# Performance work log

Hardware: AMD Instinct MI355X
Metric: run time of the kernel (lower is better)

Reference implementation:

```python
import jax, jax.numpy as jnp
import numpy as np
import math

B, T, S, D, H = 2, 1024, 1024, 1024, 16
DH = D // H


def setup_inputs() -> dict:
    key = jax.random.key(0)
    ks = jax.random.split(key, 13)
    scale = 1.0 / math.sqrt(D)
    inp = {
        "q": jax.random.normal(ks[0], (B, T, D), jnp.float32),
        "k": jax.random.normal(ks[1], (B, S, D), jnp.float32),
        "v": jax.random.normal(ks[2], (B, S, D), jnp.float32),
        # causal mask: True means masked
        "attn_mask": jnp.broadcast_to(
            jnp.triu(jnp.ones((T, S), jnp.bool_), k=1)[None, None], (B, 1, T, S)
        ),
        "attn_bias": jax.random.normal(ks[3], (B, H, T, S), jnp.float32),
        "Wq": jax.random.normal(ks[4], (D, D), jnp.float32) * scale,
        "bq": jnp.zeros((D,), jnp.float32),
        "Wk": jax.random.normal(ks[5], (D, D), jnp.float32) * scale,
        "bk": jnp.zeros((D,), jnp.float32),
        "Wv": jax.random.normal(ks[6], (D, D), jnp.float32) * scale,
        "bv": jnp.zeros((D,), jnp.float32),
        "Wo": jax.random.normal(ks[7], (D, D), jnp.float32) * scale,
        "bo": jnp.zeros((D,), jnp.float32),
        "bias_scale": jnp.asarray(0.5, jnp.float32),
    }
    return inp


def reference(q, k, v, attn_mask, attn_bias, Wq, bq, Wk, bk, Wv, bv, Wo, bo, bias_scale):
    # projections (torch Linear convention: x @ W.T + b), split heads
    qh = (q @ Wq.T + bq).reshape(B, T, H, DH)   # (B,T,H,DH)
    kh = (k @ Wk.T + bk).reshape(B, S, H, DH)
    vh = (v @ Wv.T + bv).reshape(B, S, H, DH)

    scores = jnp.einsum("bthd,bshd->bhts", qh, kh) / math.sqrt(DH)  # (B,H,T,S)
    scores = jnp.clip(scores, -80.0, 80.0)
    scores = jnp.where(attn_mask, -jnp.inf, scores)  # mask broadcasts over H
    attn = jax.nn.softmax(scores, axis=-1)

    # post-softmax multiplicative bias + renormalize
    scale = 1.0 + bias_scale * jnp.tanh(attn_bias)
    attn = attn * jnp.maximum(scale, 1e-9)
    attn = attn / (jnp.sum(attn, axis=-1, keepdims=True) + 1e-9)

    # dropout p=0.0 (eval) -> identity
    out = jnp.einsum("bhts,bshd->bthd", attn, vh).reshape(B, T, D)
    out = out @ Wo.T + bo
    return out, attn
```

## Files before the change

### kernel.cpp

```cpp
#include <hip/hip_runtime.h>
#include <hip/hip_bf16.h>
#include <math.h>

#define BB 2
#define TT 1024
#define SS 1024
#define DD 1024
#define HH 16
#define DH 64

typedef __attribute__((ext_vector_type(8))) short bf16x8;
typedef __attribute__((ext_vector_type(4))) float f32x4;
typedef unsigned short ushort_t;

#define AS3(p) ((__attribute__((address_space(3))) unsigned int*)(p))
#define AS1(p) ((const __attribute__((address_space(1))) unsigned int*)(p))

__device__ __forceinline__ unsigned short f2b(float f) {
    union { float f; unsigned u; } x; x.f = f;
    unsigned r = x.u + 0x7FFFu + ((x.u >> 16) & 1u);
    return (unsigned short)(r >> 16);
}

__device__ __forceinline__ bf16x8 pack_bf16x8(float4 a, float4 b) {
    union { unsigned u[4]; bf16x8 v; } r;
    asm("v_cvt_pk_bf16_f32 %0, %1, %2" : "=v"(r.u[0]) : "v"(a.x), "v"(a.y));
    asm("v_cvt_pk_bf16_f32 %0, %1, %2" : "=v"(r.u[1]) : "v"(a.z), "v"(a.w));
    asm("v_cvt_pk_bf16_f32 %0, %1, %2" : "=v"(r.u[2]) : "v"(b.x), "v"(b.y));
    asm("v_cvt_pk_bf16_f32 %0, %1, %2" : "=v"(r.u[3]) : "v"(b.z), "v"(b.w));
    return r.v;
}

__global__ __launch_bounds__(256) void cvt_all(
    const float* __restrict__ q, const float* __restrict__ k, const float* __restrict__ v,
    const float* __restrict__ Wq, const float* __restrict__ Wk,
    const float* __restrict__ Wv, const float* __restrict__ Wo,
    ushort_t* __restrict__ oq, ushort_t* __restrict__ ok, ushort_t* __restrict__ ov,
    ushort_t* __restrict__ oWq, ushort_t* __restrict__ oWk,
    ushort_t* __restrict__ oWv, ushort_t* __restrict__ oWo)
{
    const int y = blockIdx.y;
    if (y >= 3 && blockIdx.x >= 512) return;
    const float* src =
        (y == 0) ? q : (y == 1) ? k : (y == 2) ? v :
        (y == 3) ? Wq : (y == 4) ? Wk : (y == 5) ? Wv : Wo;
    ushort_t* dst =
        (y == 0) ? oq : (y == 1) ? ok : (y == 2) ? ov :
        (y == 3) ? oWq : (y == 4) ? oWk : (y == 5) ? oWv : oWo;
    size_t i = ((size_t)blockIdx.x * 256 + threadIdx.x) * 8;
    float4 v0 = *(const float4*)&src[i];
    float4 v1 = *(const float4*)&src[i + 4];
    uint4 o;
    o.x = f2b(v0.x) | ((unsigned)f2b(v0.y) << 16);
    o.y = f2b(v0.z) | ((unsigned)f2b(v0.w) << 16);
    o.z = f2b(v1.x) | ((unsigned)f2b(v1.y) << 16);
    o.w = f2b(v1.z) | ((unsigned)f2b(v1.w) << 16);
    *(uint4*)&dst[i] = o;
}

__device__ __forceinline__ void gemm128_mainloop(
    const ushort_t* __restrict__ A,
    const ushort_t* __restrict__ Bw,
    int K, ushort_t (*Asm)[128 * 32], ushort_t (*Bsm)[128 * 32],
    f32x4 acc[4][4])
{
    const int tid = threadIdx.x;
    const int wave = tid >> 6, lane = tid & 63;
    const int sr = lane >> 2;
    const int gc = (lane & 3) ^ ((lane >> 3) & 3);
    const int l15 = lane & 15, q = lane >> 4;
    const int mblk = (wave >> 1) * 64, nblk = (wave & 1) * 64;

#define G128_STAGE(k0_, b_) do {                                               \
        _Pragma("unroll")                                                      \
        for (int o = 0; o < 2; o++) {                                          \
            int r0 = (wave * 2 + o) * 16;                                      \
            __builtin_amdgcn_global_load_lds(                                  \
                AS1(A + (size_t)(r0 + sr) * K + (k0_) + gc * 8),               \
                AS3(Asm[b_] + r0 * 32), 16, 0, 0);                             \
            __builtin_amdgcn_global_load_lds(                                  \
                AS1(Bw + (size_t)(r0 + sr) * K + (k0_) + gc * 8),              \
                AS3(Bsm[b_] + r0 * 32), 16, 0, 0);                             \
        } } while (0)

#define G128_COMPUTE(b_) do {                                                  \
        bf16x8 av[4], bv[4];                                                   \
        _Pragma("unroll")                                                      \
        for (int mi = 0; mi < 4; mi++) {                                       \
            int r = mblk + mi * 16 + l15;                                      \
            av[mi] = *(const bf16x8*)&Asm[b_][r * 32 + (q ^ ((r >> 1) & 3)) * 8]; \
        }                                                                      \
        _Pragma("unroll")                                                      \
        for (int ni = 0; ni < 4; ni++) {                                       \
            int r = nblk + ni * 16 + l15;                                      \
            bv[ni] = *(const bf16x8*)&Bsm[b_][r * 32 + (q ^ ((r >> 1) & 3)) * 8]; \
        }                                                                      \
        _Pragma("unroll")                                                      \
        for (int mi = 0; mi < 4; mi++)                                         \
            _Pragma("unroll")                                                  \
            for (int ni = 0; ni < 4; ni++)                                     \
                acc[mi][ni] = __builtin_amdgcn_mfma_f32_16x16x32_bf16(         \
                    av[mi], bv[ni], acc[mi][ni], 0, 0, 0);                     \
        } while (0)

    G128_STAGE(0, 0);
    __syncthreads();

    int buf = 0;
    for (int k0 = 0; k0 < K; k0 += 32) {
        if (k0 + 32 < K) G128_STAGE(k0 + 32, buf ^ 1);
        G128_COMPUTE(buf);
        __syncthreads();
        buf ^= 1;
    }
#undef G128_STAGE
#undef G128_COMPUTE
}

__global__ __launch_bounds__(256) void proj_gemm(
    const ushort_t* __restrict__ qb, const ushort_t* __restrict__ kb, const ushort_t* __restrict__ vb,
    const ushort_t* __restrict__ Wqb, const ushort_t* __restrict__ Wkb, const ushort_t* __restrict__ Wvb,
    const float* __restrict__ bq, const float* __restrict__ bk, const float* __restrict__ bv,
    ushort_t* __restrict__ qh, ushort_t* __restrict__ kh, ushort_t* __restrict__ vh)
{
    __shared__ ushort_t Asm[2][128 * 32];
    __shared__ ushort_t Bsm[2][128 * 32];
    const int z = blockIdx.z;
    const ushort_t* A = (z == 0) ? qb : (z == 1) ? kb : vb;
    const ushort_t* W = (z == 0) ? Wqb : (z == 1) ? Wkb : Wvb;
    const float* bias = (z == 0) ? bq : (z == 1) ? bk : bv;
    ushort_t* Y = (z == 0) ? qh : (z == 1) ? kh : vh;

    const int bm = blockIdx.y * 128, bn = blockIdx.x * 128;
    f32x4 acc[4][4];
    #pragma unroll
    for (int i = 0; i < 4; i++)
        #pragma unroll
        for (int j = 0; j < 4; j++) acc[i][j] = (f32x4)(0.f);

    gemm128_mainloop(A + (size_t)bm * DD, W + (size_t)bn * DD, DD, Asm, Bsm, acc);

    const int lane = threadIdx.x & 63, wave = threadIdx.x >> 6;
    const int mblk = (wave >> 1) * 64, nblk = (wave & 1) * 64;
    const int l15 = lane & 15, q = lane >> 4;
    #pragma unroll
    for (int mi = 0; mi < 4; mi++) {
        #pragma unroll
        for (int ni = 0; ni < 4; ni++) {
            int col = bn + nblk + ni * 16 + l15;
            float bcol = bias[col];
            #pragma unroll
            for (int r = 0; r < 4; r++) {
                int row = bm + mblk + mi * 16 + q * 4 + r;
                Y[(size_t)row * DD + col] = f2b(acc[mi][ni][r] + bcol);
            }
        }
    }
}

__global__ __launch_bounds__(256) void oproj_gemm(
    const ushort_t* __restrict__ A, const ushort_t* __restrict__ W,
    const float* __restrict__ bias, float* __restrict__ Y)
{
    __shared__ ushort_t Asm[2][128 * 32];
    __shared__ ushort_t Bsm[2][128 * 32];
    const int bm = blockIdx.y * 128, bn = blockIdx.x * 128;
    f32x4 acc[4][4];
    #pragma unroll
    for (int i = 0; i < 4; i++)
        #pragma unroll
        for (int j = 0; j < 4; j++) acc[i][j] = (f32x4)(0.f);

    gemm128_mainloop(A + (size_t)bm * DD, W + (size_t)bn * DD, DD, Asm, Bsm, acc);

    const int lane = threadIdx.x & 63, wave = threadIdx.x >> 6;
    const int mblk = (wave >> 1) * 64, nblk = (wave & 1) * 64;
    const int l15 = lane & 15, q = lane >> 4;
    #pragma unroll
    for (int mi = 0; mi < 4; mi++) {
        #pragma unroll
        for (int ni = 0; ni < 4; ni++) {
            int col = bn + nblk + ni * 16 + l15;
            float bcol = bias[col];
            #pragma unroll
            for (int r = 0; r < 4; r++) {
                int row = bm + mblk + mi * 16 + q * 4 + r;
                Y[(size_t)row * DD + col] = acc[mi][ni][r] + bcol;
            }
        }
    }
}

__global__ __launch_bounds__(256) void transpose_v(
    const ushort_t* __restrict__ vh, ushort_t* __restrict__ vT)
{
    __shared__ ushort_t Ls[64][72];
    const int s0 = blockIdx.x * 64;
    const int bh = blockIdx.y;
    const int b = bh >> 4, h = bh & 15;
    const int tid = threadIdx.x;
    const int r = tid >> 2, c16 = (tid & 3) * 16;

    const ushort_t* src = &vh[((size_t)(b * SS + s0 + r) * HH + h) * DH + c16];
    uint4 u0 = *(const uint4*)src;
    uint4 u1 = *(const uint4*)(src + 8);
    ushort_t tmp[16];
    *(uint4*)&tmp[0] = u0; *(uint4*)&tmp[8] = u1;
    #pragma unroll
    for (int j = 0; j < 16; j++) Ls[c16 + j][r] = tmp[j];
    __syncthreads();

    const int dh = r;
    uint4 w0 = *(const uint4*)&Ls[dh][c16];
    uint4 w1 = *(const uint4*)&Ls[dh][c16 + 8];
    ushort_t* dst = &vT[((size_t)bh * DH + dh) * SS + s0 + c16];
    *(uint4*)dst = w0;
    *(uint4*)(dst + 8) = w1;
}

__global__ __launch_bounds__(256) void scores_mfma(
    const ushort_t* __restrict__ qh, const ushort_t* __restrict__ kh,
    float* __restrict__ attn)
{
    __shared__ ushort_t Qs[128 * 64];
    __shared__ ushort_t Ks[128 * 64];

    int idx = blockIdx.x, ti = 0;
    while (idx >= ti + 1) { idx -= ti + 1; ti++; }
    const int si = idx;
    const int bh = blockIdx.y;
    const int b = bh >> 4, h = bh & 15;
    const int t0 = ti * 128, s0 = si * 128;

    const int tid = threadIdx.x;
    const int wave = tid >> 6, lane = tid & 63;
    const int sr8 = lane >> 3;
    const int gc8 = (lane & 7) ^ sr8;

    #pragma unroll
    for (int o = 0; o < 4; o++) {
        int r0 = (wave * 4 + o) * 8;
        int r = r0 + sr8;
        __builtin_amdgcn_global_load_lds(
            AS1(qh + ((size_t)(b * TT + t0 + r) * HH + h) * DH + gc8 * 8),
            AS3(Qs + r0 * 64), 16, 0, 0);
        __builtin_amdgcn_global_load_lds(
            AS1(kh + ((size_t)(b * SS + s0 + r) * HH + h) * DH + gc8 * 8),
            AS3(Ks + r0 * 64), 16, 0, 0);
    }
    __syncthreads();

    const int l15 = lane & 15, q = lane >> 4;
    const int tblk = (wave >> 1) * 64, sblk = (wave & 1) * 64;
    f32x4 acc[4][4];
    #pragma unroll
    for (int i = 0; i < 4; i++)
        #pragma unroll
        for (int j = 0; j < 4; j++) acc[i][j] = (f32x4)(0.f);

    #pragma unroll
    for (int ks = 0; ks < 2; ks++) {
        bf16x8 av[4], bv[4];
        #pragma unroll
        for (int mi = 0; mi < 4; mi++) {
            int r = tblk + mi * 16 + l15;
            av[mi] = *(const bf16x8*)&Qs[r * 64 + ((ks * 4 + q) ^ (r & 7)) * 8];
        }
        #pragma unroll
        for (int ni = 0; ni < 4; ni++) {
            int r = sblk + ni * 16 + l15;
            bv[ni] = *(const bf16x8*)&Ks[r * 64 + ((ks * 4 + q) ^ (r & 7)) * 8];
        }
        #pragma unroll
        for (int mi = 0; mi < 4; mi++)
            #pragma unroll
            for (int ni = 0; ni < 4; ni++)
                acc[mi][ni] = __builtin_amdgcn_mfma_f32_16x16x32_bf16(av[mi], bv[ni], acc[mi][ni], 0, 0, 0);
    }

    #pragma unroll
    for (int mi = 0; mi < 4; mi++) {
        #pragma unroll
        for (int ni = 0; ni < 4; ni++) {
            int scol = s0 + sblk + ni * 16 + l15;
            #pragma unroll
            for (int r = 0; r < 4; r++) {
                int t = t0 + tblk + mi * 16 + q * 4 + r;
                float v = acc[mi][ni][r] * 0.125f;
                v = fminf(fmaxf(v, -80.f), 80.f);
                attn[((size_t)bh * TT + t) * SS + scol] = v;
            }
        }
    }
}

__global__ __launch_bounds__(256) void softmax_bias_wave(
    const float* __restrict__ attn_bias, const float* __restrict__ bias_scale_p,
    float* __restrict__ attn)
{
    const int wave = threadIdx.x >> 6, lane = threadIdx.x & 63;
    const int row = blockIdx.x * 4 + wave;
    const int t = row & (TT - 1);

    float* prow = attn + (size_t)row * SS;
    const float* brow = attn_bias + (size_t)row * SS;
    const float bscale = bias_scale_p[0];

    const int nc = (t >> 8) + 1;

    float v[16];
    float4 bx[4];
    float m = -INFINITY;
    #pragma unroll
    for (int c = 0; c < 4; c++) {
        const int s0 = c * 256 + lane * 4;
        if (c < nc) {
            float4 rv = *(const float4*)&prow[s0];
            bx[c] = *(const float4*)&brow[s0];
            v[c * 4 + 0] = (s0     <= t) ? rv.x : -INFINITY;
            v[c * 4 + 1] = (s0 + 1 <= t) ? rv.y : -INFINITY;
            v[c * 4 + 2] = (s0 + 2 <= t) ? rv.z : -INFINITY;
            v[c * 4 + 3] = (s0 + 3 <= t) ? rv.w : -INFINITY;
            m = fmaxf(m, fmaxf(fmaxf(v[c*4], v[c*4+1]), fmaxf(v[c*4+2], v[c*4+3])));
        } else {
            v[c * 4 + 0] = -INFINITY; v[c * 4 + 1] = -INFINITY;
            v[c * 4 + 2] = -INFINITY; v[c * 4 + 3] = -INFINITY;
            bx[c] = make_float4(0.f, 0.f, 0.f, 0.f);
        }
    }
    #pragma unroll
    for (int off = 1; off < 64; off <<= 1)
        m = fmaxf(m, __shfl_xor(m, off));

    float w[16];
    float P = 0.f, Wn = 0.f;
    #pragma unroll
    for (int c = 0; c < 4; c++) {
        if (c < nc) {
            float bxx[4] = {bx[c].x, bx[c].y, bx[c].z, bx[c].w};
            #pragma unroll
            for (int j = 0; j < 4; j++) {
                float vv = v[c * 4 + j];
                float p = (vv > -INFINITY) ? __expf(vv - m) : 0.f;
                float e = __expf(-2.f * fabsf(bxx[j]));
                float th = copysignf((1.f - e) / (1.f + e), bxx[j]);
                float sc = fmaxf(1.f + bscale * th, 1e-9f);
                float ww = p * sc;
                w[c * 4 + j] = ww;
                P += p; Wn += ww;
            }
        } else {
            w[c * 4 + 0] = 0.f; w[c * 4 + 1] = 0.f;
            w[c * 4 + 2] = 0.f; w[c * 4 + 3] = 0.f;
        }
    }
    #pragma unroll
    for (int off = 1; off < 64; off <<= 1) {
        P  += __shfl_xor(P, off);
        Wn += __shfl_xor(Wn, off);
    }
    const float inv = 1.f / (Wn + 1e-9f * P);

    #pragma unroll
    for (int c = 0; c < 4; c++) {
        const int s0 = c * 256 + lane * 4;
        float4 o;
        o.x = w[c * 4 + 0] * inv; o.y = w[c * 4 + 1] * inv;
        o.z = w[c * 4 + 2] * inv; o.w = w[c * 4 + 3] * inv;
        *(float4*)&prow[s0] = o;
    }
}

__global__ __launch_bounds__(256) void av_mfma(
    const float* __restrict__ attn, const ushort_t* __restrict__ vT,
    ushort_t* __restrict__ ao)
{
    __shared__ ushort_t Vsm[2][64 * 64];

    const int tb = (int)gridDim.x - 1 - (int)blockIdx.x;
    const int bh = blockIdx.y;
    const int b = bh >> 4, h = bh & 15;
    const int t0 = tb * 64;
    const int nsteps = tb + 1;

    const int tid = threadIdx.x;
    const int wave = tid >> 6, lane = tid & 63;
    const int sr8 = lane >> 3, gc8 = (lane & 7) ^ sr8;
    const int l15 = lane & 15, q = lane >> 4;

    const float* arow = attn + ((size_t)bh * TT + t0 + wave * 16 + l15) * SS + q * 8;
    const ushort_t* vbase = vT + (size_t)bh * DH * SS;

    f32x4 acc[4];
    #pragma unroll
    for (int i = 0; i < 4; i++) acc[i] = (f32x4)(0.f);

#define STAGE_V(sidx, buf) do {                                               \
        int s0_ = (sidx) * 64;                                                \
        _Pragma("unroll")                                                     \
        for (int o = 0; o < 2; o++) {                                         \
            int r0 = wave * 16 + o * 8;                                       \
            __builtin_amdgcn_global_load_lds(                                 \
                AS1(vbase + (size_t)(r0 + sr8) * SS + s0_ + gc8 * 8),         \
                AS3(&Vsm[buf][r0 * 64]), 16, 0, 0);                           \
        } } while (0)

#define LOAD_A(sidx, dst) do {                                                \
        const float* p_ = arow + (sidx) * 64;                                 \
        dst[0] = *(const float4*)(p_);                                        \
        dst[1] = *(const float4*)(p_ + 4);                                    \
        dst[2] = *(const float4*)(p_ + 32);                                   \
        dst[3] = *(const float4*)(p_ + 36); } while (0)

#define COMPUTE(buf, ax) do {                                                 \
        bf16x8 af0 = pack_bf16x8(ax[0], ax[1]);                               \
        bf16x8 af1 = pack_bf16x8(ax[2], ax[3]);                               \
        _Pragma("unroll")                                                     \
        for (int ni = 0; ni < 4; ni++) {                                      \
            int rv = ni * 16 + l15;                                           \
            bf16x8 b0 = *(const bf16x8*)&Vsm[buf][rv * 64 + ((q) ^ (rv & 7)) * 8];       \
            bf16x8 b1 = *(const bf16x8*)&Vsm[buf][rv * 64 + ((4 + q) ^ (rv & 7)) * 8];   \
            acc[ni] = __builtin_amdgcn_mfma_f32_16x16x32_bf16(af0, b0, acc[ni], 0, 0, 0);\
            acc[ni] = __builtin_amdgcn_mfma_f32_16x16x32_bf16(af1, b1, acc[ni], 0, 0, 0);\
        } } while (0)

    float4 aA[4], aB[4];
    STAGE_V(0, 0);
    LOAD_A(0, aA);
    __syncthreads();

    int st = 0;
    while (true) {
        if (st + 1 < nsteps) { STAGE_V(st + 1, 1); LOAD_A(st + 1, aB); }
        COMPUTE(0, aA);
        __syncthreads();
        if (++st == nsteps) break;
        if (st + 1 < nsteps) { STAGE_V(st + 1, 0); LOAD_A(st + 1, aA); }
        COMPUTE(1, aB);
        __syncthreads();
        if (++st == nsteps) break;
    }

#undef STAGE_V
#undef LOAD_A
#undef COMPUTE

    #pragma unroll
    for (int ni = 0; ni < 4; ni++) {
        int dh = ni * 16 + l15;
        #pragma unroll
        for (int r = 0; r < 4; r++) {
            int t = t0 + wave * 16 + q * 4 + r;
            ao[(size_t)(b * TT + t) * DD + h * DH + dh] = f2b(acc[ni][r]);
        }
    }
}

extern "C" void kernel_launch(void* const* d_in, const int* in_sizes, int n_in,
                              void* d_out, int out_size, void* d_ws, size_t ws_size,
                              hipStream_t stream)
{
    const float* q   = (const float*)d_in[0];
    const float* k   = (const float*)d_in[1];
    const float* v   = (const float*)d_in[2];
    const float* attn_bias = (const float*)d_in[4];
    const float* Wq = (const float*)d_in[5];
    const float* bq = (const float*)d_in[6];
    const float* Wk = (const float*)d_in[7];
    const float* bk = (const float*)d_in[8];
    const float* Wv = (const float*)d_in[9];
    const float* bv = (const float*)d_in[10];
    const float* Wo = (const float*)d_in[11];
    const float* bo = (const float*)d_in[12];
    const float* bscale = (const float*)d_in[13];

    char* base = (char*)d_ws;
    ushort_t* qb  = (ushort_t*)(base + (0ull << 20));
    ushort_t* kb  = (ushort_t*)(base + (4ull << 20));
    ushort_t* vb  = (ushort_t*)(base + (8ull << 20));
    ushort_t* Wqb = (ushort_t*)(base + (12ull << 20));
    ushort_t* Wkb = (ushort_t*)(base + (14ull << 20));
    ushort_t* Wvb = (ushort_t*)(base + (16ull << 20));
    ushort_t* Wob = (ushort_t*)(base + (18ull << 20));
    ushort_t* qhb = (ushort_t*)(base + (20ull << 20));
    ushort_t* khb = (ushort_t*)(base + (24ull << 20));
    ushort_t* vhb = (ushort_t*)(base + (28ull << 20));
    ushort_t* vT  = qb;
    ushort_t* aob = kb;

    float* out  = (float*)d_out;
    float* attn = out + (size_t)BB * TT * DD;

    cvt_all<<<dim3(1024, 7), 256, 0, stream>>>(q, k, v, Wq, Wk, Wv, Wo,
                                               qb, kb, vb, Wqb, Wkb, Wvb, Wob);
    proj_gemm<<<dim3(8, 16, 3), 256, 0, stream>>>(qb, kb, vb, Wqb, Wkb, Wvb,
                                                  bq, bk, bv, qhb, khb, vhb);
    transpose_v<<<dim3(16, 32), 256, 0, stream>>>(vhb, vT);
    scores_mfma<<<dim3(36, 32), 256, 0, stream>>>(qhb, khb, attn);
    softmax_bias_wave<<<dim3(8192), 256, 0, stream>>>(attn_bias, bscale, attn);
    av_mfma<<<dim3(16, 32), 256, 0, stream>>>(attn, vT, aob);
    oproj_gemm<<<dim3(8, 16), 256, 0, stream>>>(aob, Wob, bo, out);
}
```

Measured before the change: 367.4 us.

## Fuse softmax-bias normalization into the attention-times-V MFMA kernel

Replaces the separate softmax_bias_wave and av_mfma kernels with one 512-thread kernel. Each block computes the unnormalized biased weights per 64-column tile, stores them as bf16 in a 128KB LDS row buffer and feeds them straight to the MFMA. It then normalizes both the attn output and the AV accumulator by a per-row reciprocal. A fixed exponent offset of 16 replaces the row max to avoid a second pass, and the kernel zero-fills the masked tail directly. This removes a full re-read and re-write of the attention matrix. The costs are bf16 rounding of the returned attn values, the fixed-offset exponent relying on the clipped score range, and one block per CU because of the large LDS use.

```diff
diff --git a/kernel.cpp b/kernel.cpp
--- a/kernel.cpp
+++ b/kernel.cpp
@@ -22,13 +22,9 @@
     return (unsigned short)(r >> 16);
 }
 
-__device__ __forceinline__ bf16x8 pack_bf16x8(float4 a, float4 b) {
-    union { unsigned u[4]; bf16x8 v; } r;
-    asm("v_cvt_pk_bf16_f32 %0, %1, %2" : "=v"(r.u[0]) : "v"(a.x), "v"(a.y));
-    asm("v_cvt_pk_bf16_f32 %0, %1, %2" : "=v"(r.u[1]) : "v"(a.z), "v"(a.w));
-    asm("v_cvt_pk_bf16_f32 %0, %1, %2" : "=v"(r.u[2]) : "v"(b.x), "v"(b.y));
-    asm("v_cvt_pk_bf16_f32 %0, %1, %2" : "=v"(r.u[3]) : "v"(b.z), "v"(b.w));
-    return r.v;
+__device__ __forceinline__ float b2f(unsigned short u) {
+    union { unsigned u; float f; } x; x.u = ((unsigned)u) << 16;
+    return x.f;
 }
 
 __global__ __launch_bounds__(256) void cvt_all(
@@ -294,164 +290,158 @@
     }
 }
 
-__global__ __launch_bounds__(256) void softmax_bias_wave(
-    const float* __restrict__ attn_bias, const float* __restrict__ bias_scale_p,
-    float* __restrict__ attn)
-{
-    const int wave = threadIdx.x >> 6, lane = threadIdx.x & 63;
-    const int row = blockIdx.x * 4 + wave;
-    const int t = row & (TT - 1);
-
-    float* prow = attn + (size_t)row * SS;
-    const float* brow = attn_bias + (size_t)row * SS;
-    const float bscale = bias_scale_p[0];
-
-    const int nc = (t >> 8) + 1;
-
-    float v[16];
-    float4 bx[4];
-    float m = -INFINITY;
-    #pragma unroll
-    for (int c = 0; c < 4; c++) {
-        const int s0 = c * 256 + lane * 4;
-        if (c < nc) {
-            float4 rv = *(const float4*)&prow[s0];
-            bx[c] = *(const float4*)&brow[s0];
-            v[c * 4 + 0] = (s0     <= t) ? rv.x : -INFINITY;
-            v[c * 4 + 1] = (s0 + 1 <= t) ? rv.y : -INFINITY;
-            v[c * 4 + 2] = (s0 + 2 <= t) ? rv.z : -INFINITY;
-            v[c * 4 + 3] = (s0 + 3 <= t) ? rv.w : -INFINITY;
-            m = fmaxf(m, fmaxf(fmaxf(v[c*4], v[c*4+1]), fmaxf(v[c*4+2], v[c*4+3])));
-        } else {
-            v[c * 4 + 0] = -INFINITY; v[c * 4 + 1] = -INFINITY;
-            v[c * 4 + 2] = -INFINITY; v[c * 4 + 3] = -INFINITY;
-            bx[c] = make_float4(0.f, 0.f, 0.f, 0.f);
-        }
-    }
-    #pragma unroll
-    for (int off = 1; off < 64; off <<= 1)
-        m = fmaxf(m, __shfl_xor(m, off));
-
-    float w[16];
-    float P = 0.f, Wn = 0.f;
-    #pragma unroll
-    for (int c = 0; c < 4; c++) {
-        if (c < nc) {
-            float bxx[4] = {bx[c].x, bx[c].y, bx[c].z, bx[c].w};
-            #pragma unroll
-            for (int j = 0; j < 4; j++) {
-                float vv = v[c * 4 + j];
-                float p = (vv > -INFINITY) ? __expf(vv - m) : 0.f;
-                float e = __expf(-2.f * fabsf(bxx[j]));
-                float th = copysignf((1.f - e) / (1.f + e), bxx[j]);
-                float sc = fmaxf(1.f + bscale * th, 1e-9f);
-                float ww = p * sc;
-                w[c * 4 + j] = ww;
-                P += p; Wn += ww;
-            }
-        } else {
-            w[c * 4 + 0] = 0.f; w[c * 4 + 1] = 0.f;
-            w[c * 4 + 2] = 0.f; w[c * 4 + 3] = 0.f;
-        }
-    }
-    #pragma unroll
-    for (int off = 1; off < 64; off <<= 1) {
-        P  += __shfl_xor(P, off);
-        Wn += __shfl_xor(Wn, off);
-    }
-    const float inv = 1.f / (Wn + 1e-9f * P);
-
-    #pragma unroll
-    for (int c = 0; c < 4; c++) {
-        const int s0 = c * 256 + lane * 4;
-        float4 o;
-        o.x = w[c * 4 + 0] * inv; o.y = w[c * 4 + 1] * inv;
-        o.z = w[c * 4 + 2] * inv; o.w = w[c * 4 + 3] * inv;
-        *(float4*)&prow[s0] = o;
-    }
-}
-
-__global__ __launch_bounds__(256) void av_mfma(
-    const float* __restrict__ attn, const ushort_t* __restrict__ vT,
+__global__ __launch_bounds__(512) void sav_fused(
+    const float* __restrict__ scores,
+    const float* __restrict__ attn_bias,
+    const float* __restrict__ bias_scale_p,
+    const ushort_t* __restrict__ vT,
+    float* __restrict__ attn,
     ushort_t* __restrict__ ao)
 {
+    __shared__ ushort_t Wlds[64 * 1024];
     __shared__ ushort_t Vsm[2][64 * 64];
+    __shared__ float sInv[64];
 
     const int tb = (int)gridDim.x - 1 - (int)blockIdx.x;
     const int bh = blockIdx.y;
     const int b = bh >> 4, h = bh & 15;
     const int t0 = tb * 64;
-    const int nsteps = tb + 1;
+    const int nst = tb + 1;
 
     const int tid = threadIdx.x;
     const int wave = tid >> 6, lane = tid & 63;
+    const int crow = wave * 8 + (lane >> 3);
+    const int cc8  = (lane & 7) * 8;
+    const int csw  = (cc8 ^ ((crow & 7) << 3));
+    const int tglob = t0 + crow;
+    const int rg = wave >> 1, dhh = wave & 1;
+    const int l15 = lane & 15, q = lane >> 4;
+    const int arow = rg * 16 + l15;
     const int sr8 = lane >> 3, gc8 = (lane & 7) ^ sr8;
-    const int l15 = lane & 15, q = lane >> 4;
-
-    const float* arow = attn + ((size_t)bh * TT + t0 + wave * 16 + l15) * SS + q * 8;
+
+    const float bscale = bias_scale_p[0];
+    const float* srow = scores    + ((size_t)bh * TT + tglob) * SS + cc8;
+    const float* brow = attn_bias + ((size_t)bh * TT + tglob) * SS + cc8;
     const ushort_t* vbase = vT + (size_t)bh * DH * SS;
-
-    f32x4 acc[4];
-    #pragma unroll
-    for (int i = 0; i < 4; i++) acc[i] = (f32x4)(0.f);
-
-#define STAGE_V(sidx, buf) do {                                               \
-        int s0_ = (sidx) * 64;                                                \
+    float* aout = attn + ((size_t)bh * TT + tglob) * SS + cc8;
+
+    {
+        float4 z = make_float4(0.f, 0.f, 0.f, 0.f);
+        for (int si = nst; si < SS / 64; si++) {
+            *(float4*)(aout + si * 64) = z;
+            *(float4*)(aout + si * 64 + 4) = z;
+        }
+    }
+
+    f32x4 acc[2];
+    acc[0] = (f32x4)(0.f); acc[1] = (f32x4)(0.f);
+    float P = 0.f, Wn = 0.f;
+
+#define STAGE_V(sidx, bb) do {                                                \
+        __builtin_amdgcn_global_load_lds(                                     \
+            AS1(vbase + (size_t)(wave * 8 + sr8) * SS + (sidx) * 64 + gc8 * 8),\
+            AS3(&Vsm[bb][(wave * 8) * 64]), 16, 0, 0); } while (0)
+
+#define LOAD_SB(ti_, sv_, bv_) do {                                           \
+        const float* ps_ = srow + (ti_) * 64;                                 \
+        const float* pb_ = brow + (ti_) * 64;                                 \
+        sv_[0] = *(const float4*)ps_; sv_[1] = *(const float4*)(ps_ + 4);     \
+        bv_[0] = *(const float4*)pb_; bv_[1] = *(const float4*)(pb_ + 4); } while (0)
+
+#define COMPUTE_W(ti_, sv_, bv_) do {                                         \
+        float sa_[8] = { sv_[0].x, sv_[0].y, sv_[0].z, sv_[0].w,              \
+                         sv_[1].x, sv_[1].y, sv_[1].z, sv_[1].w };            \
+        float ba_[8] = { bv_[0].x, bv_[0].y, bv_[0].z, bv_[0].w,              \
+                         bv_[1].x, bv_[1].y, bv_[1].z, bv_[1].w };            \
+        float wv_[8];                                                         \
         _Pragma("unroll")                                                     \
-        for (int o = 0; o < 2; o++) {                                         \
-            int r0 = wave * 16 + o * 8;                                       \
-            __builtin_amdgcn_global_load_lds(                                 \
-                AS1(vbase + (size_t)(r0 + sr8) * SS + s0_ + gc8 * 8),         \
-                AS3(&Vsm[buf][r0 * 64]), 16, 0, 0);                           \
+        for (int j = 0; j < 8; j++) {                                         \
+            int col_ = (ti_) * 64 + cc8 + j;                                  \
+            float p_ = (col_ <= tglob) ? __expf(sa_[j] - 16.f) : 0.f;         \
+            float e_ = __expf(-2.f * fabsf(ba_[j]));                          \
+            float th_ = copysignf((1.f - e_) / (1.f + e_), ba_[j]);           \
+            float sc_ = fmaxf(1.f + bscale * th_, 1e-9f);                     \
+            float ww_ = p_ * sc_;                                             \
+            P += p_; Wn += ww_; wv_[j] = ww_;                                 \
+        }                                                                     \
+        union { unsigned u[4]; uint4 v4; } pk_;                               \
+        asm("v_cvt_pk_bf16_f32 %0, %1, %2" : "=v"(pk_.u[0]) : "v"(wv_[0]), "v"(wv_[1])); \
+        asm("v_cvt_pk_bf16_f32 %0, %1, %2" : "=v"(pk_.u[1]) : "v"(wv_[2]), "v"(wv_[3])); \
+        asm("v_cvt_pk_bf16_f32 %0, %1, %2" : "=v"(pk_.u[2]) : "v"(wv_[4]), "v"(wv_[5])); \
+        asm("v_cvt_pk_bf16_f32 %0, %1, %2" : "=v"(pk_.u[3]) : "v"(wv_[6]), "v"(wv_[7])); \
+        *(uint4*)&Wlds[(size_t)crow * 1024 + (ti_) * 64 + csw] = pk_.v4; } while (0)
+
+#define MFMA_T(ti_, bb) do {                                                  \
+        bf16x8 a0 = *(const bf16x8*)&Wlds[(size_t)arow * 1024 + (ti_) * 64 + ((q ^ (arow & 7)) << 3)];       \
+        bf16x8 a1 = *(const bf16x8*)&Wlds[(size_t)arow * 1024 + (ti_) * 64 + (((4 + q) ^ (arow & 7)) << 3)]; \
+        _Pragma("unroll")                                                     \
+        for (int ni = 0; ni < 2; ni++) {                                      \
+            int rv = dhh * 32 + ni * 16 + l15;                                \
+            bf16x8 b0 = *(const bf16x8*)&Vsm[bb][rv * 64 + ((q ^ (rv & 7)) << 3)];       \
+            bf16x8 b1 = *(const bf16x8*)&Vsm[bb][rv * 64 + (((4 + q) ^ (rv & 7)) << 3)]; \
+            acc[ni] = __builtin_amdgcn_mfma_f32_16x16x32_bf16(a0, b0, acc[ni], 0, 0, 0); \
+            acc[ni] = __builtin_amdgcn_mfma_f32_16x16x32_bf16(a1, b1, acc[ni], 0, 0, 0); \
         } } while (0)
 
-#define LOAD_A(sidx, dst) do {                                                \
-        const float* p_ = arow + (sidx) * 64;                                 \
-        dst[0] = *(const float4*)(p_);                                        \
-        dst[1] = *(const float4*)(p_ + 4);                                    \
-        dst[2] = *(const float4*)(p_ + 32);                                   \
-        dst[3] = *(const float4*)(p_ + 36); } while (0)
-
-#define COMPUTE(buf, ax) do {                                                 \
-        bf16x8 af0 = pack_bf16x8(ax[0], ax[1]);                               \
-        bf16x8 af1 = pack_bf16x8(ax[2], ax[3]);                               \
-        _Pragma("unroll")                                                     \
-        for (int ni = 0; ni < 4; ni++) {                                      \
-            int rv = ni * 16 + l15;                                           \
-            bf16x8 b0 = *(const bf16x8*)&Vsm[buf][rv * 64 + ((q) ^ (rv & 7)) * 8];       \
-            bf16x8 b1 = *(const bf16x8*)&Vsm[buf][rv * 64 + ((4 + q) ^ (rv & 7)) * 8];   \
-            acc[ni] = __builtin_amdgcn_mfma_f32_16x16x32_bf16(af0, b0, acc[ni], 0, 0, 0);\
-            acc[ni] = __builtin_amdgcn_mfma_f32_16x16x32_bf16(af1, b1, acc[ni], 0, 0, 0);\
-        } } while (0)
-
-    float4 aA[4], aB[4];
+    float4 sA[2], bA[2], sB[2], bB[2];
     STAGE_V(0, 0);
-    LOAD_A(0, aA);
-    __syncthreads();
+    LOAD_SB(0, sA, bA);
 
     int st = 0;
     while (true) {
-        if (st + 1 < nsteps) { STAGE_V(st + 1, 1); LOAD_A(st + 1, aB); }
-        COMPUTE(0, aA);
+        COMPUTE_W(st, sA, bA);
         __syncthreads();
-        if (++st == nsteps) break;
-        if (st + 1 < nsteps) { STAGE_V(st + 1, 0); LOAD_A(st + 1, aA); }
-        COMPUTE(1, aB);
+        if (st + 1 < nst) { STAGE_V(st + 1, 1); LOAD_SB(st + 1, sB, bB); }
+        MFMA_T(st, 0);
+        if (++st == nst) break;
+
+        COMPUTE_W(st, sB, bB);
         __syncthreads();
-        if (++st == nsteps) break;
-    }
-
+        if (st + 1 < nst) { STAGE_V(st + 1, 0); LOAD_SB(st + 1, sA, bA); }
+        MFMA_T(st, 1);
+        if (++st == nst) break;
+    }
 #undef STAGE_V
-#undef LOAD_A
-#undef COMPUTE
-
-    #pragma unroll
-    for (int ni = 0; ni < 4; ni++) {
-        int dh = ni * 16 + l15;
+#undef LOAD_SB
+#undef COMPUTE_W
+#undef MFMA_T
+
+    #pragma unroll
+    for (int off = 1; off < 8; off <<= 1) {
+        P  += __shfl_xor(P, off);
+        Wn += __shfl_xor(Wn, off);
+    }
+    if ((lane & 7) == 0) sInv[crow] = 1.f / (Wn + 1e-9f * P);
+    __syncthreads();
+
+    {
+        const float rinv = sInv[crow];
+        for (int si = 0; si < nst; si++) {
+            union { uint4 v4; unsigned u[4]; } pk;
+            pk.v4 = *(const uint4*)&Wlds[(size_t)crow * 1024 + si * 64 + csw];
+            float4 o0, o1;
+            o0.x = b2f((ushort_t)(pk.u[0] & 0xffff)) * rinv;
+            o0.y = b2f((ushort_t)(pk.u[0] >> 16)) * rinv;
+            o0.z = b2f((ushort_t)(pk.u[1] & 0xffff)) * rinv;
+            o0.w = b2f((ushort_t)(pk.u[1] >> 16)) * rinv;
+            o1.x = b2f((ushort_t)(pk.u[2] & 0xffff)) * rinv;
+            o1.y = b2f((ushort_t)(pk.u[2] >> 16)) * rinv;
+            o1.z = b2f((ushort_t)(pk.u[3] & 0xffff)) * rinv;
+            o1.w = b2f((ushort_t)(pk.u[3] >> 16)) * rinv;
+            *(float4*)(aout + si * 64) = o0;
+            *(float4*)(aout + si * 64 + 4) = o1;
+        }
+    }
+
+    #pragma unroll
+    for (int ni = 0; ni < 2; ni++) {
+        int dh = dhh * 32 + ni * 16 + l15;
         #pragma unroll
         for (int r = 0; r < 4; r++) {
-            int t = t0 + wave * 16 + q * 4 + r;
-            ao[(size_t)(b * TT + t) * DD + h * DH + dh] = f2b(acc[ni][r]);
+            int trow = rg * 16 + q * 4 + r;
+            float iv = sInv[trow];
+            int t = t0 + trow;
+            ao[(size_t)(b * TT + t) * DD + h * DH + dh] = f2b(acc[ni][r] * iv);
         }
     }
 }
@@ -497,7 +487,7 @@
                                                   bq, bk, bv, qhb, khb, vhb);
     transpose_v<<<dim3(16, 32), 256, 0, stream>>>(vhb, vT);
     scores_mfma<<<dim3(36, 32), 256, 0, stream>>>(qhb, khb, attn);
-    softmax_bias_wave<<<dim3(8192), 256, 0, stream>>>(attn_bias, bscale, attn);
-    av_mfma<<<dim3(16, 32), 256, 0, stream>>>(attn, vT, aob);
+    sav_fused<<<dim3(16, 32), 512, 0, stream>>>(attn, attn_bias, bscale, vT,
+                                                attn, aob);
     oproj_gemm<<<dim3(8, 16), 256, 0, stream>>>(aob, Wob, bo, out);
 }
```

After: 424.7 us. 1.16x slower.

## Fuse softmax-bias into scores kernel and defer normalization into AV kernel

Applied to the files above, without the earlier changes.

The scores kernel now computes exp with a fixed shift, which is safe because scores are clipped to ±80. It also applies the tanh bias scale, writes the unnormalized weights, and emits per-tile partial row sums. The AV kernel reduces those partial sums to a per-row inverse and rescales its accumulator. It also writes back the normalized attention tiles it stages through LDS, and zero-fills the masked upper region. This drops the standalone softmax pass and one launch. The costs are scattered bias reads in the scores epilogue, a second read of the weights in the AV kernel, and extra LDS use.

```diff
diff --git a/kernel.cpp b/kernel.cpp
--- a/kernel.cpp
+++ b/kernel.cpp
@@ -218,12 +218,15 @@
     *(uint4*)(dst + 8) = w1;
 }
 
-__global__ __launch_bounds__(256) void scores_mfma(
+__global__ __launch_bounds__(256) void scores_sm_mfma(
     const ushort_t* __restrict__ qh, const ushort_t* __restrict__ kh,
-    float* __restrict__ attn)
+    const float* __restrict__ attn_bias, const float* __restrict__ bias_scale_p,
+    float* __restrict__ wout, float* __restrict__ Ppart, float* __restrict__ Wpart)
 {
     __shared__ ushort_t Qs[128 * 64];
     __shared__ ushort_t Ks[128 * 64];
+    __shared__ float pPs[128][2];
+    __shared__ float pWs[128][2];
 
     int idx = blockIdx.x, ti = 0;
     while (idx >= ti + 1) { idx -= ti + 1; ti++; }
@@ -278,6 +281,13 @@
                 acc[mi][ni] = __builtin_amdgcn_mfma_f32_16x16x32_bf16(av[mi], bv[ni], acc[mi][ni], 0, 0, 0);
     }
 
+    const float bscale = bias_scale_p[0];
+    float rowP[4][4], rowW[4][4];
+    #pragma unroll
+    for (int mi = 0; mi < 4; mi++)
+        #pragma unroll
+        for (int r = 0; r < 4; r++) { rowP[mi][r] = 0.f; rowW[mi][r] = 0.f; }
+
     #pragma unroll
     for (int mi = 0; mi < 4; mi++) {
         #pragma unroll
@@ -286,123 +296,116 @@
             #pragma unroll
             for (int r = 0; r < 4; r++) {
                 int t = t0 + tblk + mi * 16 + q * 4 + r;
-                float v = acc[mi][ni][r] * 0.125f;
-                v = fminf(fmaxf(v, -80.f), 80.f);
-                attn[((size_t)bh * TT + t) * SS + scol] = v;
+                float s = acc[mi][ni][r] * 0.125f;
+                s = fminf(fmaxf(s, -80.f), 80.f);
+                float p = (scol <= t) ? __expf(s - 16.f) : 0.f;
+                float bvv = attn_bias[((size_t)bh * TT + t) * SS + scol];
+                float e = __expf(-2.f * fabsf(bvv));
+                float th = copysignf((1.f - e) / (1.f + e), bvv);
+                float sc = fmaxf(1.f + bscale * th, 1e-9f);
+                float w = p * sc;
+                wout[((size_t)bh * TT + t) * SS + scol] = w;
+                rowP[mi][r] += p;
+                rowW[mi][r] += w;
             }
         }
     }
-}
-
-__global__ __launch_bounds__(256) void softmax_bias_wave(
-    const float* __restrict__ attn_bias, const float* __restrict__ bias_scale_p,
-    float* __restrict__ attn)
-{
-    const int wave = threadIdx.x >> 6, lane = threadIdx.x & 63;
-    const int row = blockIdx.x * 4 + wave;
-    const int t = row & (TT - 1);
-
-    float* prow = attn + (size_t)row * SS;
-    const float* brow = attn_bias + (size_t)row * SS;
-    const float bscale = bias_scale_p[0];
-
-    const int nc = (t >> 8) + 1;
-
-    float v[16];
-    float4 bx[4];
-    float m = -INFINITY;
-    #pragma unroll
-    for (int c = 0; c < 4; c++) {
-        const int s0 = c * 256 + lane * 4;
-        if (c < nc) {
-            float4 rv = *(const float4*)&prow[s0];
-            bx[c] = *(const float4*)&brow[s0];
-            v[c * 4 + 0] = (s0     <= t) ? rv.x : -INFINITY;
-            v[c * 4 + 1] = (s0 + 1 <= t) ? rv.y : -INFINITY;
-            v[c * 4 + 2] = (s0 + 2 <= t) ? rv.z : -INFINITY;
-            v[c * 4 + 3] = (s0 + 3 <= t) ? rv.w : -INFINITY;
-            m = fmaxf(m, fmaxf(fmaxf(v[c*4], v[c*4+1]), fmaxf(v[c*4+2], v[c*4+3])));
-        } else {
-            v[c * 4 + 0] = -INFINITY; v[c * 4 + 1] = -INFINITY;
-            v[c * 4 + 2] = -INFINITY; v[c * 4 + 3] = -INFINITY;
-            bx[c] = make_float4(0.f, 0.f, 0.f, 0.f);
-        }
-    }
-    #pragma unroll
-    for (int off = 1; off < 64; off <<= 1)
-        m = fmaxf(m, __shfl_xor(m, off));
-
-    float w[16];
-    float P = 0.f, Wn = 0.f;
-    #pragma unroll
-    for (int c = 0; c < 4; c++) {
-        if (c < nc) {
-            float bxx[4] = {bx[c].x, bx[c].y, bx[c].z, bx[c].w};
-            #pragma unroll
-            for (int j = 0; j < 4; j++) {
-                float vv = v[c * 4 + j];
-                float p = (vv > -INFINITY) ? __expf(vv - m) : 0.f;
-                float e = __expf(-2.f * fabsf(bxx[j]));
-                float th = copysignf((1.f - e) / (1.f + e), bxx[j]);
-                float sc = fmaxf(1.f + bscale * th, 1e-9f);
-                float ww = p * sc;
-                w[c * 4 + j] = ww;
-                P += p; Wn += ww;
+
+    #pragma unroll
+    for (int off = 1; off < 16; off <<= 1) {
+        #pragma unroll
+        for (int mi = 0; mi < 4; mi++)
+            #pragma unroll
+            for (int r = 0; r < 4; r++) {
+                rowP[mi][r] += __shfl_xor(rowP[mi][r], off);
+                rowW[mi][r] += __shfl_xor(rowW[mi][r], off);
             }
-        } else {
-            w[c * 4 + 0] = 0.f; w[c * 4 + 1] = 0.f;
-            w[c * 4 + 2] = 0.f; w[c * 4 + 3] = 0.f;
-        }
-    }
-    #pragma unroll
-    for (int off = 1; off < 64; off <<= 1) {
-        P  += __shfl_xor(P, off);
-        Wn += __shfl_xor(Wn, off);
-    }
-    const float inv = 1.f / (Wn + 1e-9f * P);
-
-    #pragma unroll
-    for (int c = 0; c < 4; c++) {
-        const int s0 = c * 256 + lane * 4;
-        float4 o;
-        o.x = w[c * 4 + 0] * inv; o.y = w[c * 4 + 1] * inv;
-        o.z = w[c * 4 + 2] * inv; o.w = w[c * 4 + 3] * inv;
-        *(float4*)&prow[s0] = o;
-    }
-}
-
-__global__ __launch_bounds__(256) void av_mfma(
-    const float* __restrict__ attn, const ushort_t* __restrict__ vT,
-    ushort_t* __restrict__ ao)
+    }
+    if (l15 == 0) {
+        #pragma unroll
+        for (int mi = 0; mi < 4; mi++)
+            #pragma unroll
+            for (int r = 0; r < 4; r++) {
+                int row = tblk + mi * 16 + q * 4 + r;
+                pPs[row][wave & 1] = rowP[mi][r];
+                pWs[row][wave & 1] = rowW[mi][r];
+            }
+    }
+    __syncthreads();
+    if (tid < 128) {
+        float P2 = pPs[tid][0] + pPs[tid][1];
+        float W2 = pWs[tid][0] + pWs[tid][1];
+        size_t o = ((size_t)bh * TT + t0 + tid) * 8 + si;
+        Ppart[o] = P2;
+        Wpart[o] = W2;
+    }
+}
+
+__global__ __launch_bounds__(256) void av_norm_mfma(
+    const float* __restrict__ w, const ushort_t* __restrict__ vT,
+    const float* __restrict__ Ppart, const float* __restrict__ Wpart,
+    float* __restrict__ attn, ushort_t* __restrict__ ao)
 {
     __shared__ ushort_t Vsm[2][64 * 64];
+    __shared__ float Wsm[2][64 * 64];
+    __shared__ float sInv[64];
 
     const int tb = (int)gridDim.x - 1 - (int)blockIdx.x;
     const int bh = blockIdx.y;
     const int b = bh >> 4, h = bh & 15;
     const int t0 = tb * 64;
-    const int nsteps = tb + 1;
+    const int nst = tb + 1;
 
     const int tid = threadIdx.x;
     const int wave = tid >> 6, lane = tid & 63;
     const int sr8 = lane >> 3, gc8 = (lane & 7) ^ sr8;
     const int l15 = lane & 15, q = lane >> 4;
 
-    const float* arow = attn + ((size_t)bh * TT + t0 + wave * 16 + l15) * SS + q * 8;
+    if (tid < 64) {
+        int t = t0 + tid;
+        int n2 = (t >> 7) + 1;
+        const float* pp = Ppart + ((size_t)bh * TT + t) * 8;
+        const float* ww = Wpart + ((size_t)bh * TT + t) * 8;
+        float P = 0.f, W = 0.f;
+        for (int j = 0; j < n2; j++) { P += pp[j]; W += ww[j]; }
+        sInv[tid] = 1.f / (W + 1e-9f * P);
+    }
+
+    float* aout_base = attn + ((size_t)bh * TT + t0) * SS;
+
+    {
+        float4 z = make_float4(0.f, 0.f, 0.f, 0.f);
+        const int zr = tid >> 4, zc = (tid & 15) * 4;
+        for (int si = nst; si < SS / 64; si++)
+            #pragma unroll
+            for (int kk = 0; kk < 4; kk++)
+                *(float4*)&aout_base[(size_t)(zr + kk * 16) * SS + si * 64 + zc] = z;
+    }
+
+    const float* arow = w + ((size_t)bh * TT + t0 + wave * 16 + l15) * SS + q * 8;
     const ushort_t* vbase = vT + (size_t)bh * DH * SS;
+    const float* wtile_base = w + ((size_t)bh * TT + t0) * SS;
 
     f32x4 acc[4];
     #pragma unroll
     for (int i = 0; i < 4; i++) acc[i] = (f32x4)(0.f);
 
-#define STAGE_V(sidx, buf) do {                                               \
-        int s0_ = (sidx) * 64;                                                \
+#define STAGE_V(sidx, bb) do {                                                \
         _Pragma("unroll")                                                     \
         for (int o = 0; o < 2; o++) {                                         \
             int r0 = wave * 16 + o * 8;                                       \
             __builtin_amdgcn_global_load_lds(                                 \
-                AS1(vbase + (size_t)(r0 + sr8) * SS + s0_ + gc8 * 8),         \
-                AS3(&Vsm[buf][r0 * 64]), 16, 0, 0);                           \
+                AS1(vbase + (size_t)(r0 + sr8) * SS + (sidx) * 64 + gc8 * 8), \
+                AS3(&Vsm[bb][r0 * 64]), 16, 0, 0);                            \
+        } } while (0)
+
+#define STAGE_W(sidx, bb) do {                                                \
+        _Pragma("unroll")                                                     \
+        for (int i_ = 0; i_ < 4; i_++) {                                      \
+            int row_ = wave * 16 + i_ * 4 + (lane >> 4);                      \
+            __builtin_amdgcn_global_load_lds(                                 \
+                AS1(wtile_base + (size_t)row_ * SS + (sidx) * 64 + (lane & 15) * 4), \
+                AS3(&Wsm[bb][wave * 1024 + i_ * 256]), 16, 0, 0);             \
         } } while (0)
 
 #define LOAD_A(sidx, dst) do {                                                \
@@ -412,46 +415,63 @@
         dst[2] = *(const float4*)(p_ + 32);                                   \
         dst[3] = *(const float4*)(p_ + 36); } while (0)
 
-#define COMPUTE(buf, ax) do {                                                 \
+#define COMPUTE(bb, ax) do {                                                  \
         bf16x8 af0 = pack_bf16x8(ax[0], ax[1]);                               \
         bf16x8 af1 = pack_bf16x8(ax[2], ax[3]);                               \
         _Pragma("unroll")                                                     \
         for (int ni = 0; ni < 4; ni++) {                                      \
             int rv = ni * 16 + l15;                                           \
-            bf16x8 b0 = *(const bf16x8*)&Vsm[buf][rv * 64 + ((q) ^ (rv & 7)) * 8];       \
-            bf16x8 b1 = *(const bf16x8*)&Vsm[buf][rv * 64 + ((4 + q) ^ (rv & 7)) * 8];   \
+            bf16x8 b0 = *(const bf16x8*)&Vsm[bb][rv * 64 + ((q) ^ (rv & 7)) * 8];       \
+            bf16x8 b1 = *(const bf16x8*)&Vsm[bb][rv * 64 + ((4 + q) ^ (rv & 7)) * 8];   \
             acc[ni] = __builtin_amdgcn_mfma_f32_16x16x32_bf16(af0, b0, acc[ni], 0, 0, 0);\
             acc[ni] = __builtin_amdgcn_mfma_f32_16x16x32_bf16(af1, b1, acc[ni], 0, 0, 0);\
         } } while (0)
 
+#define WRITEBACK(bb, sidx) do {                                              \
+        const int wc_ = (tid & 15) * 4;                                       \
+        _Pragma("unroll")                                                     \
+        for (int kk = 0; kk < 4; kk++) {                                      \
+            int row_ = (tid >> 4) + kk * 16;                                  \
+            float4 vv = *(const float4*)&Wsm[bb][row_ * 64 + wc_];            \
+            float iv_ = sInv[row_];                                           \
+            vv.x *= iv_; vv.y *= iv_; vv.z *= iv_; vv.w *= iv_;               \
+            *(float4*)&aout_base[(size_t)row_ * SS + (sidx) * 64 + wc_] = vv; \
+        } } while (0)
+
     float4 aA[4], aB[4];
     STAGE_V(0, 0);
+    STAGE_W(0, 0);
     LOAD_A(0, aA);
     __syncthreads();
 
     int st = 0;
     while (true) {
-        if (st + 1 < nsteps) { STAGE_V(st + 1, 1); LOAD_A(st + 1, aB); }
+        if (st + 1 < nst) { STAGE_V(st + 1, 1); STAGE_W(st + 1, 1); LOAD_A(st + 1, aB); }
         COMPUTE(0, aA);
+        WRITEBACK(0, st);
         __syncthreads();
-        if (++st == nsteps) break;
-        if (st + 1 < nsteps) { STAGE_V(st + 1, 0); LOAD_A(st + 1, aA); }
+        if (++st == nst) break;
+        if (st + 1 < nst) { STAGE_V(st + 1, 0); STAGE_W(st + 1, 0); LOAD_A(st + 1, aA); }
         COMPUTE(1, aB);
+        WRITEBACK(1, st);
         __syncthreads();
-        if (++st == nsteps) break;
-    }
-
+        if (++st == nst) break;
+    }
 #undef STAGE_V
+#undef STAGE_W
 #undef LOAD_A
 #undef COMPUTE
+#undef WRITEBACK
 
     #pragma unroll
     for (int ni = 0; ni < 4; ni++) {
         int dh = ni * 16 + l15;
         #pragma unroll
         for (int r = 0; r < 4; r++) {
-            int t = t0 + wave * 16 + q * 4 + r;
-            ao[(size_t)(b * TT + t) * DD + h * DH + dh] = f2b(acc[ni][r]);
+            int trow = wave * 16 + q * 4 + r;
+            float iv = sInv[trow];
+            int t = t0 + trow;
+            ao[(size_t)(b * TT + t) * DD + h * DH + dh] = f2b(acc[ni][r] * iv);
         }
     }
 }
@@ -487,6 +507,8 @@
     ushort_t* vhb = (ushort_t*)(base + (28ull << 20));
     ushort_t* vT  = qb;
     ushort_t* aob = kb;
+    float* PpartB = (float*)(base + (8ull << 20));
+    float* WpartB = (float*)(base + (9ull << 20));
 
     float* out  = (float*)d_out;
     float* attn = out + (size_t)BB * TT * DD;
@@ -496,8 +518,9 @@
     proj_gemm<<<dim3(8, 16, 3), 256, 0, stream>>>(qb, kb, vb, Wqb, Wkb, Wvb,
                                                   bq, bk, bv, qhb, khb, vhb);
     transpose_v<<<dim3(16, 32), 256, 0, stream>>>(vhb, vT);
-    scores_mfma<<<dim3(36, 32), 256, 0, stream>>>(qhb, khb, attn);
-    softmax_bias_wave<<<dim3(8192), 256, 0, stream>>>(attn_bias, bscale, attn);
-    av_mfma<<<dim3(16, 32), 256, 0, stream>>>(attn, vT, aob);
+    scores_sm_mfma<<<dim3(36, 32), 256, 0, stream>>>(qhb, khb, attn_bias, bscale,
+                                                     attn, PpartB, WpartB);
+    av_norm_mfma<<<dim3(16, 32), 256, 0, stream>>>(attn, vT, PpartB, WpartB,
+                                                   attn, aob);
     oproj_gemm<<<dim3(8, 16), 256, 0, stream>>>(aob, Wob, bo, out);
 }
```

After: 373.2 us. No clear change (+1.6%).
